# Optimization experiments

Hardware: AMD Instinct MI355X
Metric: run time of the kernel (lower is better)

Reference implementation:

```python
import jax, jax.numpy as jnp
import numpy as np

N_NODES = 100000
N_EDGES = 1600000
D_IN = 128
HID = 128
N_CLS = 10
N_GRAPHS = 128


def _gcn_conv(x, W, b, src, dst, dis, n):
    # x' = W x; out[i] = sum_{(j->i)} d_j^{-1/2} d_i^{-1/2} x'_j ; then + bias
    h = x @ W  # [N, out]
    norm = dis[src] * dis[dst]  # [E_tot]
    msg = h[src] * norm[:, None]  # gather + scale (irregular access)
    out = jax.ops.segment_sum(msg, dst, num_segments=n)  # scatter-add
    return out + b


def setup_inputs() -> dict:
    key = jax.random.key(0)
    ks = jax.random.split(key, 12)
    x = jax.random.normal(ks[0], (N_NODES, D_IN), dtype=jnp.float32)
    edge_index = jax.random.randint(ks[1], (2, N_EDGES), 0, N_NODES, dtype=jnp.int64)
    batch = jnp.sort(jax.random.randint(ks[2], (N_NODES,), 0, N_GRAPHS, dtype=jnp.int64))
    drop_u = jax.random.uniform(ks[3], (N_NODES, D_IN), dtype=jnp.float32)
    s = lambda k, sh, fan: jax.random.normal(k, sh, dtype=jnp.float32) / np.sqrt(fan)
    return {
        "x": x, "edge_index": edge_index, "batch": batch, "num_graphs": N_GRAPHS,
        "drop_u": drop_u,
        "lin1_w": s(ks[4], (D_IN, D_IN), D_IN), "lin1_b": jnp.zeros((D_IN,), jnp.float32),
        "conv1_w": s(ks[5], (D_IN, HID), D_IN), "conv1_b": jnp.zeros((HID,), jnp.float32),
        "conv2_w": s(ks[6], (HID, HID // 2), HID), "conv2_b": jnp.zeros((HID // 2,), jnp.float32),
        "lin2_w": s(ks[7], (HID // 2, N_CLS), HID // 2), "lin2_b": jnp.zeros((N_CLS,), jnp.float32),
    }


def reference(x, edge_index, batch, num_graphs, drop_u,
              lin1_w, lin1_b, conv1_w, conv1_b, conv2_w, conv2_b, lin2_w, lin2_b):
    n = x.shape[0]
    # add self loops (PyG GCNConv default)
    loop = jnp.arange(n, dtype=edge_index.dtype)
    src = jnp.concatenate([edge_index[0], loop])
    dst = jnp.concatenate([edge_index[1], loop])
    deg = jax.ops.segment_sum(jnp.ones_like(dst, dtype=x.dtype), dst, num_segments=n)
    dis = jnp.where(deg > 0, jax.lax.rsqrt(deg), 0.0)  # deg^{-1/2}

    h = x @ lin1_w + lin1_b
    h = _gcn_conv(h, conv1_w, conv1_b, src, dst, dis, n)
    # dropout p=0.5 (training mode in original): keep where u >= 0.5, scale by 2
    h = h * (drop_u >= 0.5).astype(h.dtype) * 2.0
    h = jax.nn.relu(h)
    h = _gcn_conv(h, conv2_w, conv2_b, src, dst, dis, n)
    # global mean pool over graph ids
    sums = jax.ops.segment_sum(h, batch, num_segments=num_graphs)
    cnts = jax.ops.segment_sum(jnp.ones((n,), h.dtype), batch, num_segments=num_graphs)
    pooled = sums / jnp.maximum(cnts, 1.0)[:, None]
    return pooled @ lin2_w + lin2_b
```

## Files before the change

### kernel.cpp

```cpp
#include <hip/hip_runtime.h>
#include <hip/hip_bf16.h>

#define DIN   128
#define HID2  64
#define NCLS  10
#define NGRAPH 128
#define SCAN_CHUNK 1024
#define NBLK 256
#define NBKT_MAX 512
#define CAP 6144

typedef __attribute__((ext_vector_type(8))) short bf16x8;
typedef __attribute__((ext_vector_type(4))) float f32x4;

__device__ __forceinline__ void atomAddF(float* p, float v) {
    unsafeAtomicAdd(p, v);
}

__device__ __forceinline__ unsigned short f2bf(float f) {
    unsigned int u = __float_as_uint(f);
    u += 0x7fffu + ((u >> 16) & 1u);
    return (unsigned short)(u >> 16);
}

__global__ __launch_bounds__(128) void k_w12(const float* __restrict__ lw,
                                             const float* __restrict__ lb,
                                             const float* __restrict__ cw,
                                             const float* __restrict__ cw2,
                                             float* __restrict__ W12,
                                             float* __restrict__ c1preb,
                                             unsigned short* __restrict__ w2b) {
    int i = blockIdx.x, j = threadIdx.x;
    if (i == 129) {
        for (int f = j; f < 8192; f += 128) w2b[f] = f2bf(cw2[(f & 127) * 64 + (f >> 7)]);
        return;
    }
    const float* arow = (i < 128) ? (lw + i * 128) : lb;
    float acc = 0.f;
#pragma unroll 8
    for (int k = 0; k < 128; ++k) acc += arow[k] * cw[k * 128 + j];
    if (i < 128) W12[i * 128 + j] = acc;
    else         c1preb[j] = acc;
}

__global__ __launch_bounds__(256) void k_bhist(const int* __restrict__ dst,
                                               int* __restrict__ bh, int E, int nbkt,
                                               float* __restrict__ zbuf, int zn) {
    __shared__ int lh[NBKT_MAX];
    if (blockIdx.x == 0)
        for (int i = threadIdx.x; i < zn; i += 256) zbuf[i] = 0.f;
    for (int i = threadIdx.x; i < nbkt; i += 256) lh[i] = 0;
    __syncthreads();
    for (int e = blockIdx.x * 256 + threadIdx.x; e < E; e += NBLK * 256)
        atomicAdd(&lh[__builtin_nontemporal_load(dst + e) >> 8], 1);
    __syncthreads();
    for (int i = threadIdx.x; i < nbkt; i += 256) bh[i * NBLK + blockIdx.x] = lh[i];
}

__global__ __launch_bounds__(256) void k_scan_part(const int* __restrict__ cnt,
                                                   int* __restrict__ part, int n) {
    int base = blockIdx.x * SCAN_CHUNK + threadIdx.x * 4;
    int s = 0;
#pragma unroll
    for (int j = 0; j < 4; ++j) { int i = base + j; if (i < n) s += cnt[i]; }
#pragma unroll
    for (int o = 32; o > 0; o >>= 1) s += __shfl_down(s, o);
    __shared__ int wsum[4];
    if ((threadIdx.x & 63) == 0) wsum[threadIdx.x >> 6] = s;
    __syncthreads();
    if (threadIdx.x == 0) part[blockIdx.x] = wsum[0] + wsum[1] + wsum[2] + wsum[3];
}
__global__ __launch_bounds__(256) void k_scan_mid(int* __restrict__ part,
                                                  int* __restrict__ total_out,
                                                  int B, int n) {
    __shared__ int sh[256];
    int t = threadIdx.x;
    int v = (t < B) ? part[t] : 0;
    sh[t] = v;
    __syncthreads();
    for (int off = 1; off < 256; off <<= 1) {
        int u = (t >= off) ? sh[t - off] : 0;
        __syncthreads();
        sh[t] += u;
        __syncthreads();
    }
    if (t < B) part[t] = sh[t] - v;
    if (t == 255) total_out[n] = sh[255];
}
__global__ __launch_bounds__(256) void k_scan_fin2(const int* cnt,
                                                   const int* __restrict__ part,
                                                   int* out, int n) {
    __shared__ int sh[256];
    int t = threadIdx.x;
    int base = blockIdx.x * SCAN_CHUNK + t * 4;
    int c[4]; int s = 0;
#pragma unroll
    for (int j = 0; j < 4; ++j) { int i = base + j; c[j] = (i < n) ? cnt[i] : 0; s += c[j]; }
    sh[t] = s;
    __syncthreads();
    for (int off = 1; off < 256; off <<= 1) {
        int u = (t >= off) ? sh[t - off] : 0;
        __syncthreads();
        sh[t] += u;
        __syncthreads();
    }
    int excl = part[blockIdx.x] + sh[t] - s;
#pragma unroll
    for (int j = 0; j < 4; ++j) {
        int i = base + j;
        if (i < n) out[i] = excl;
        excl += c[j];
    }
}

__global__ __launch_bounds__(256) void k_partition(const int* __restrict__ src,
                                                   const int* __restrict__ dst,
                                                   const int* __restrict__ bh,
                                                   int* __restrict__ pairs, int E, int nbkt) {
    __shared__ int cur[NBKT_MAX];
    for (int i = threadIdx.x; i < nbkt; i += 256) cur[i] = bh[i * NBLK + blockIdx.x];
    __syncthreads();
    for (int e = blockIdx.x * 256 + threadIdx.x; e < E; e += NBLK * 256) {
        int d = __builtin_nontemporal_load(dst + e);
        int s = __builtin_nontemporal_load(src + e);
        int pos = atomicAdd(&cur[d >> 8], 1);
        pairs[pos] = (s << 8) | (d & 255);
    }
}

__global__ __launch_bounds__(256) void k_csr_local(const int* __restrict__ pairs,
                                                   const int* __restrict__ bh,
                                                   int* __restrict__ row_start,
                                                   float* __restrict__ dis,
                                                   int* __restrict__ col,
                                                   int N) {
    __shared__ int cntL[256], scanL[256], curL[256];
    __shared__ int srcbuf[CAP];
    const int tid = threadIdx.x;
    const int lo = blockIdx.x << 8;
    const int bstart = bh[blockIdx.x * NBLK];
    const int bend = bh[(blockIdx.x + 1) * NBLK];
    const int nE = bend - bstart;

    cntL[tid] = 0;
    __syncthreads();
    for (int e = bstart + tid; e < bend; e += 256)
        atomicAdd(&cntL[pairs[e] & 255], 1);
    __syncthreads();
    const int deg = cntL[tid];
    scanL[tid] = deg;
    __syncthreads();
    for (int off = 1; off < 256; off <<= 1) {
        int u = (tid >= off) ? scanL[tid - off] : 0;
        __syncthreads();
        scanL[tid] += u;
        __syncthreads();
    }
    const int excl = scanL[tid] - deg;
    curL[tid] = excl;
    const int node = lo + tid;
    if (node < N) {
        row_start[node] = bstart + excl;
        dis[node] = rsqrtf((float)(deg + 1));
    } else if (node == N) {
        row_start[N] = bend;
    }
    __syncthreads();
    if (nE <= CAP) {
        for (int e = bstart + tid; e < bend; e += 256) {
            int p = pairs[e];
            int pos = atomicAdd(&curL[p & 255], 1);
            srcbuf[pos] = ((unsigned int)p) >> 8;
        }
        __syncthreads();
        for (int i = tid; i < nE; i += 256)
            col[bstart + i] = srcbuf[i];
    } else {
        for (int e = bstart + tid; e < bend; e += 256) {
            int p = pairs[e];
            int pos = atomicAdd(&curL[p & 255], 1);
            col[bstart + pos] = ((unsigned int)p) >> 8;
        }
    }
}

__global__ __launch_bounds__(256) void k_mask(const float* __restrict__ du,
                                              unsigned int* __restrict__ dmask, int nw) {
    const int w = blockIdx.x * 256 + threadIdx.x;
    if (w >= nw) return;
    const float* p = du + (size_t)w * 32;
    unsigned int m = 0;
#pragma unroll
    for (int j = 0; j < 8; ++j) {
        const float4 v = *(const float4*)(p + j * 4);
        m |= (v.x >= 0.5f ? 1u : 0u) << (j * 4 + 0);
        m |= (v.y >= 0.5f ? 1u : 0u) << (j * 4 + 1);
        m |= (v.z >= 0.5f ? 1u : 0u) << (j * 4 + 2);
        m |= (v.w >= 0.5f ? 1u : 0u) << (j * 4 + 3);
    }
    dmask[w] = m;
}

template <int NCOL>
__global__ __launch_bounds__(256) void k_gemm_mfma(const float* __restrict__ A,
                                                   const float* __restrict__ W,
                                                   const float* __restrict__ bias,
                                                   unsigned short* __restrict__ out, int M) {
    constexpr int KP = 136;
    __shared__ unsigned short As[64 * KP];
    __shared__ unsigned short Wt[NCOL * KP];

    const int tid = threadIdx.x;
    const int row0 = blockIdx.x * 64;

    for (int f = tid; f < 2048; f += 256) {
        int r = f >> 5, c4 = f & 31;
        int gr = row0 + r;
        float4 v = make_float4(0.f, 0.f, 0.f, 0.f);
        if (gr < M) v = *(const float4*)(A + (size_t)gr * 128 + c4 * 4);
        ushort4 b;
        b.x = f2bf(v.x); b.y = f2bf(v.y); b.z = f2bf(v.z); b.w = f2bf(v.w);
        *(ushort4*)(&As[r * KP + c4 * 4]) = b;
    }
    for (int f = tid; f < 32 * NCOL; f += 256) {
        int k = f / (NCOL / 4), n4 = f % (NCOL / 4);
        float4 v = *(const float4*)(W + (size_t)k * NCOL + n4 * 4);
        Wt[(n4 * 4 + 0) * KP + k] = f2bf(v.x);
        Wt[(n4 * 4 + 1) * KP + k] = f2bf(v.y);
        Wt[(n4 * 4 + 2) * KP + k] = f2bf(v.z);
        Wt[(n4 * 4 + 3) * KP + k] = f2bf(v.w);
    }
    __syncthreads();

    const int wave = tid >> 6, lane = tid & 63;
    const int quad = lane >> 4, l16 = lane & 15;
    constexpr int CT = (NCOL == 128) ? 2 : 1;
    const int col0 = wave * 16 * CT;

    f32x4 acc[4][CT];
#pragma unroll
    for (int rt = 0; rt < 4; ++rt)
#pragma unroll
        for (int ct = 0; ct < CT; ++ct) acc[rt][ct] = 0.f;

#pragma unroll
    for (int ks = 0; ks < 4; ++ks) {
        const int kbase = ks * 32 + quad * 8;
        bf16x8 bfr[CT];
#pragma unroll
        for (int ct = 0; ct < CT; ++ct)
            bfr[ct] = *(const bf16x8*)(&Wt[(col0 + ct * 16 + l16) * KP + kbase]);
#pragma unroll
        for (int rt = 0; rt < 4; ++rt) {
            bf16x8 afr = *(const bf16x8*)(&As[(rt * 16 + l16) * KP + kbase]);
#pragma unroll
            for (int ct = 0; ct < CT; ++ct)
                acc[rt][ct] = __builtin_amdgcn_mfma_f32_16x16x32_bf16(afr, bfr[ct], acc[rt][ct], 0, 0, 0);
        }
    }

#pragma unroll
    for (int rt = 0; rt < 4; ++rt)
#pragma unroll
        for (int ct = 0; ct < CT; ++ct) {
            const int c = col0 + ct * 16 + l16;
            const float bv = bias ? bias[c] : 0.f;
#pragma unroll
            for (int reg = 0; reg < 4; ++reg) {
                const int gr = row0 + rt * 16 + quad * 4 + reg;
                if (gr < M) out[(size_t)gr * NCOL + c] = f2bf(acc[rt][ct][reg] + bv);
            }
        }
}

__device__ __forceinline__ void bfacc(uint4 v, float d, float* acc) {
    acc[0] = fmaf(d, __uint_as_float(v.x << 16),        acc[0]);
    acc[1] = fmaf(d, __uint_as_float(v.x & 0xffff0000u), acc[1]);
    acc[2] = fmaf(d, __uint_as_float(v.y << 16),        acc[2]);
    acc[3] = fmaf(d, __uint_as_float(v.y & 0xffff0000u), acc[3]);
    acc[4] = fmaf(d, __uint_as_float(v.z << 16),        acc[4]);
    acc[5] = fmaf(d, __uint_as_float(v.z & 0xffff0000u), acc[5]);
    acc[6] = fmaf(d, __uint_as_float(v.w << 16),        acc[6]);
    acc[7] = fmaf(d, __uint_as_float(v.w & 0xffff0000u), acc[7]);
}

__global__ __launch_bounds__(256) void k_gather_gemm2(const unsigned short* __restrict__ h,
                                                      const int* __restrict__ row_start,
                                                      const int* __restrict__ col,
                                                      const float* __restrict__ dis,
                                                      const float* __restrict__ bias,
                                                      const unsigned int* __restrict__ dmask,
                                                      const unsigned short* __restrict__ w2b,
                                                      unsigned short* __restrict__ h2b,
                                                      int n) {
    constexpr int KP = 136;
    __shared__ unsigned short As[16 * KP];
    __shared__ unsigned short Wt[64 * KP];
    const int tid = threadIdx.x;
    const int node0 = blockIdx.x * 16;
    const int node = node0 + (tid >> 4);
    const int l = tid & 15;
    const int coff = l * 8;

    for (int f = tid * 4; f < 8192; f += 1024) {
        const int c = f >> 7, k = f & 127;
        *(ushort4*)(&Wt[c * KP + k]) = *(const ushort4*)(&w2b[f]);
    }

    float r[8];
    if (node < n) {
        const float dn = dis[node];
        const unsigned int mword = dmask[node * 4 + (l >> 2)];
        const unsigned int mbyte = (mword >> ((l & 3) * 8)) & 0xffu;
        float acc[8];
        {
            uint4 v = *(const uint4*)(h + (size_t)node * 128 + coff);
#pragma unroll
            for (int q = 0; q < 8; ++q) acc[q] = 0.f;
            bfacc(v, dn, acc);
        }
        const int beg = row_start[node], end = row_start[node + 1];
        int j = beg;
        for (; j + 3 < end; j += 4) {
            const int s0 = col[j], s1 = col[j + 1], s2 = col[j + 2], s3 = col[j + 3];
            const float d0 = dis[s0], d1 = dis[s1], d2 = dis[s2], d3 = dis[s3];
            const uint4 v0 = *(const uint4*)(h + (size_t)s0 * 128 + coff);
            const uint4 v1 = *(const uint4*)(h + (size_t)s1 * 128 + coff);
            const uint4 v2 = *(const uint4*)(h + (size_t)s2 * 128 + coff);
            const uint4 v3 = *(const uint4*)(h + (size_t)s3 * 128 + coff);
            bfacc(v0, d0, acc);
            bfacc(v1, d1, acc);
            bfacc(v2, d2, acc);
            bfacc(v3, d3, acc);
        }
        for (; j < end; ++j) {
            const int s0 = col[j];
            const float d0 = dis[s0];
            const uint4 v0 = *(const uint4*)(h + (size_t)s0 * 128 + coff);
            bfacc(v0, d0, acc);
        }
        const float4 b0 = *(const float4*)(bias + coff);
        const float4 b1 = *(const float4*)(bias + coff + 4);
        r[0] = fmaf(dn, acc[0], b0.x); r[1] = fmaf(dn, acc[1], b0.y);
        r[2] = fmaf(dn, acc[2], b0.z); r[3] = fmaf(dn, acc[3], b0.w);
        r[4] = fmaf(dn, acc[4], b1.x); r[5] = fmaf(dn, acc[5], b1.y);
        r[6] = fmaf(dn, acc[6], b1.z); r[7] = fmaf(dn, acc[7], b1.w);
#pragma unroll
        for (int q = 0; q < 8; ++q)
            r[q] = ((mbyte >> q) & 1u) ? 2.f * fmaxf(r[q], 0.f) : 0.f;
    } else {
#pragma unroll
        for (int q = 0; q < 8; ++q) r[q] = 0.f;
    }
    ushort4 o0, o1;
    o0.x = f2bf(r[0]); o0.y = f2bf(r[1]); o0.z = f2bf(r[2]); o0.w = f2bf(r[3]);
    o1.x = f2bf(r[4]); o1.y = f2bf(r[5]); o1.z = f2bf(r[6]); o1.w = f2bf(r[7]);
    *(ushort4*)(&As[(tid >> 4) * KP + coff]) = o0;
    *(ushort4*)(&As[(tid >> 4) * KP + coff + 4]) = o1;
    __syncthreads();

    const int wave = tid >> 6, lane = tid & 63;
    const int quad = lane >> 4, l16 = lane & 15;
    const int c0 = wave * 16;
    f32x4 a2 = 0.f;
#pragma unroll
    for (int ks = 0; ks < 4; ++ks) {
        const int kbase = ks * 32 + quad * 8;
        bf16x8 afr = *(const bf16x8*)(&As[l16 * KP + kbase]);
        bf16x8 bfr = *(const bf16x8*)(&Wt[(c0 + l16) * KP + kbase]);
        a2 = __builtin_amdgcn_mfma_f32_16x16x32_bf16(afr, bfr, a2, 0, 0, 0);
    }
#pragma unroll
    for (int reg = 0; reg < 4; ++reg) {
        const int gr = node0 + quad * 4 + reg;
        if (gr < n) h2b[(size_t)gr * 64 + c0 + l16] = f2bf(a2[reg]);
    }
}

__global__ __launch_bounds__(256) void k_gather_pool(const unsigned short* __restrict__ h,
                                                     const int* __restrict__ row_start,
                                                     const int* __restrict__ col,
                                                     const float* __restrict__ dis,
                                                     const float* __restrict__ bias,
                                                     const int* __restrict__ batch,
                                                     float* __restrict__ partial,
                                                     int* __restrict__ bgid,
                                                     int* __restrict__ bvcnt,
                                                     float* __restrict__ sums,
                                                     float* __restrict__ cnt, int n) {
    __shared__ float bsum[4][64];
    __shared__ int sh_gfirst, sh_uni;
    const int tid = threadIdx.x;
    const int node = (blockIdx.x * 256 + tid) >> 3;
    const int l = tid & 7;
    const int coff = l * 8;
    const bool valid = node < n;
    const int node0 = blockIdx.x * 32;

    if (tid == 0) { sh_gfirst = batch[node0]; sh_uni = 1; }
    __syncthreads();
    const int gfirst = sh_gfirst;

    float r[8];
    int g = gfirst;
    if (valid) {
        const float dn = dis[node];
        g = batch[node];
        float acc[8];
        {
            uint4 v = *(const uint4*)(h + (size_t)node * 64 + coff);
#pragma unroll
            for (int q = 0; q < 8; ++q) acc[q] = 0.f;
            bfacc(v, dn, acc);
        }
        const int beg = row_start[node], end = row_start[node + 1];
        int j = beg;
        for (; j + 3 < end; j += 4) {
            const int s0 = col[j], s1 = col[j + 1], s2 = col[j + 2], s3 = col[j + 3];
            const float d0 = dis[s0], d1 = dis[s1], d2 = dis[s2], d3 = dis[s3];
            const uint4 v0 = *(const uint4*)(h + (size_t)s0 * 64 + coff);
            const uint4 v1 = *(const uint4*)(h + (size_t)s1 * 64 + coff);
            const uint4 v2 = *(const uint4*)(h + (size_t)s2 * 64 + coff);
            const uint4 v3 = *(const uint4*)(h + (size_t)s3 * 64 + coff);
            bfacc(v0, d0, acc);
            bfacc(v1, d1, acc);
            bfacc(v2, d2, acc);
            bfacc(v3, d3, acc);
        }
        for (; j < end; ++j) {
            const int s0 = col[j];
            const float d0 = dis[s0];
            const uint4 v0 = *(const uint4*)(h + (size_t)s0 * 64 + coff);
            bfacc(v0, d0, acc);
        }
        const float4 b0 = *(const float4*)(bias + coff);
        const float4 b1 = *(const float4*)(bias + coff + 4);
        r[0] = fmaf(dn, acc[0], b0.x); r[1] = fmaf(dn, acc[1], b0.y);
        r[2] = fmaf(dn, acc[2], b0.z); r[3] = fmaf(dn, acc[3], b0.w);
        r[4] = fmaf(dn, acc[4], b1.x); r[5] = fmaf(dn, acc[5], b1.y);
        r[6] = fmaf(dn, acc[6], b1.z); r[7] = fmaf(dn, acc[7], b1.w);
    } else {
#pragma unroll
        for (int q = 0; q < 8; ++q) r[q] = 0.f;
    }

    if (valid && g != gfirst) atomicAnd(&sh_uni, 0);
    __syncthreads();

    if (sh_uni) {
#pragma unroll
        for (int q = 0; q < 8; ++q) {
            r[q] += __shfl_xor(r[q], 8);
            r[q] += __shfl_xor(r[q], 16);
            r[q] += __shfl_xor(r[q], 32);
        }
        const int wave = tid >> 6, lane = tid & 63;
        if (lane < 8) {
#pragma unroll
            for (int q = 0; q < 8; ++q) bsum[wave][lane * 8 + q] = r[q];
        }
        __syncthreads();
        if (tid < 64)
            partial[(size_t)blockIdx.x * 64 + tid] =
                bsum[0][tid] + bsum[1][tid] + bsum[2][tid] + bsum[3][tid];
        if (tid == 0) {
            bgid[blockIdx.x] = gfirst;
            bvcnt[blockIdx.x] = min(n - node0, 32);
        }
    } else {
        if (tid == 0) bgid[blockIdx.x] = -1;
        const int g0 = __shfl(g, 0);
        const bool wuni = __all(valid && (g == g0));
        if (wuni) {
#pragma unroll
            for (int q = 0; q < 8; ++q) {
                r[q] += __shfl_xor(r[q], 8);
                r[q] += __shfl_xor(r[q], 16);
                r[q] += __shfl_xor(r[q], 32);
            }
            const int lane = tid & 63;
            if (lane < 8) {
#pragma unroll
                for (int q = 0; q < 8; ++q) atomAddF(&sums[g0 * 64 + lane * 8 + q], r[q]);
                if (lane == 0) atomAddF(&cnt[g0], 8.0f);
            }
        } else if (valid) {
#pragma unroll
            for (int q = 0; q < 8; ++q) atomAddF(&sums[g * 64 + coff + q], r[q]);
            if (l == 0) atomAddF(&cnt[g], 1.0f);
        }
    }
}

__global__ __launch_bounds__(256) void k_pool2(const float* __restrict__ partial,
                                               const int* __restrict__ bgid,
                                               const int* __restrict__ bvcnt,
                                               float* __restrict__ sums,
                                               float* __restrict__ cnt, int nb) {
    const int grp = (blockIdx.x * 256 + (int)threadIdx.x) >> 6;
    const int f = threadIdx.x & 63;
    const int ngroups = gridDim.x * 4;
    const int per = (nb + ngroups - 1) / ngroups;
    const int start = grp * per, end = min(nb, start + per);
    if (start >= end) return;
    int cg = -1;
    float acc = 0.f;
    int vc = 0;
    for (int b = start; b < end; ++b) {
        const int g = bgid[b];
        if (g != cg) {
            if (cg >= 0) {
                atomAddF(&sums[cg * 64 + f], acc);
                if (f == 0) atomAddF(&cnt[cg], (float)vc);
            }
            acc = 0.f; vc = 0; cg = g;
        }
        if (g >= 0) {
            acc += partial[(size_t)b * 64 + f];
            vc += bvcnt[b];
        }
    }
    if (cg >= 0) {
        atomAddF(&sums[cg * 64 + f], acc);
        if (f == 0) atomAddF(&cnt[cg], (float)vc);
    }
}

__global__ __launch_bounds__(64) void k_final(const float* __restrict__ sums,
                                              const float* __restrict__ cnt,
                                              const float* __restrict__ w,
                                              const float* __restrict__ b,
                                              float* __restrict__ out) {
    int g = blockIdx.x, f = threadIdx.x;
    float c = fmaxf(cnt[g], 1.0f);
    float p = sums[g * 64 + f] / c;
#pragma unroll
    for (int cls = 0; cls < NCLS; ++cls) {
        float v = p * w[f * 10 + cls];
#pragma unroll
        for (int o = 32; o > 0; o >>= 1) v += __shfl_down(v, o);
        if (f == 0) out[g * 10 + cls] = v + b[cls];
    }
}

extern "C" void kernel_launch(void* const* d_in, const int* in_sizes, int n_in,
                              void* d_out, int out_size, void* d_ws, size_t ws_size,
                              hipStream_t stream) {
    const float* x       = (const float*)d_in[0];
    const int*   ei      = (const int*)d_in[1];
    const int*   batch   = (const int*)d_in[2];
    const float* drop_u  = (const float*)d_in[4];
    const float* lin1_w  = (const float*)d_in[5];
    const float* lin1_b  = (const float*)d_in[6];
    const float* conv1_w = (const float*)d_in[7];
    const float* conv1_b = (const float*)d_in[8];
    const float* conv2_w = (const float*)d_in[9];
    const float* conv2_b = (const float*)d_in[10];
    const float* lin2_w  = (const float*)d_in[11];
    const float* lin2_b  = (const float*)d_in[12];
    float* out = (float*)d_out;

    const int N = in_sizes[0] / DIN;
    const int E = in_sizes[1] / 2;
    const int* src = ei;
    const int* dst = ei + E;

    const int nbkt = (N + 255) >> 8;
    const int M = nbkt * NBLK;
    const int nbGP = (int)(((size_t)N * 8 + 255) / 256);

    float* ws    = (float*)d_ws;
    float* out1  = ws;
    unsigned short* h1b = (unsigned short*)(ws + (size_t)N * 128);
    float* dis   = ws + (size_t)N * 128 + (size_t)N * 64;
    float* W12   = dis + N;
    float* c1pb  = W12 + 16384;
    float* sums  = c1pb + 128;
    float* cntp  = sums + NGRAPH * 64;
    int*   row_start = (int*)(cntp + NGRAPH);
    int*   part  = row_start + N + 2;
    int*   bh    = part + 256;
    int*   col   = bh + NBKT_MAX * NBLK + 2;
    int*   pairs = col + E;
    float* partial = (float*)(pairs + E);
    int*   bgid  = (int*)(partial + (size_t)nbGP * 64);
    int*   bvcnt = bgid + nbGP;
    unsigned int* dmask = (unsigned int*)pairs;
    unsigned short* h2b = (unsigned short*)out1;
    unsigned short* w2b = (unsigned short*)(out1 + (size_t)N * 64);

    k_w12<<<130, 128, 0, stream>>>(lin1_w, lin1_b, conv1_w, conv2_w, W12, c1pb, w2b);

    k_bhist<<<NBLK, 256, 0, stream>>>(dst, bh, E, nbkt, sums, NGRAPH * 64 + NGRAPH);
    const int scanB = (M + SCAN_CHUNK - 1) / SCAN_CHUNK;
    k_scan_part<<<scanB, 256, 0, stream>>>(bh, part, M);
    k_scan_mid<<<1, 256, 0, stream>>>(part, bh, scanB, M);
    k_scan_fin2<<<scanB, 256, 0, stream>>>(bh, part, bh, M);
    k_partition<<<NBLK, 256, 0, stream>>>(src, dst, bh, pairs, E, nbkt);
    k_csr_local<<<nbkt, 256, 0, stream>>>(pairs, bh, row_start, dis, col, N);

    k_mask<<<(N * 4 + 255) / 256, 256, 0, stream>>>(drop_u, dmask, N * 4);

    const int gemmGrid = (N + 63) / 64;
    k_gemm_mfma<128><<<gemmGrid, 256, 0, stream>>>(x, W12, c1pb, h1b, N);

    k_gather_gemm2<<<(N + 15) / 16, 256, 0, stream>>>(h1b, row_start, col, dis, conv1_b,
                                                      dmask, w2b, h2b, N);

    k_gather_pool<<<nbGP, 256, 0, stream>>>(h2b, row_start, col, dis, conv2_b, batch,
                                            partial, bgid, bvcnt, sums, cntp, N);
    k_pool2<<<16, 256, 0, stream>>>(partial, bgid, bvcnt, sums, cntp, nbGP);

    k_final<<<NGRAPH, 64, 0, stream>>>(sums, cntp, lin2_w, lin2_b, out);
}
```

Measured before the change: 379.3 us.

## Fuse weight prep into histogram, mask into GEMM, and stage partition in LDS

The W12/bias/W2 weight-precompute kernel is folded into extra blocks of the bucket-histogram launch, and the dropout-mask packing is folded into the first MFMA GEMM's load phase. Together these remove two kernel launches. The partition kernel now recomputes a per-block local histogram, scans it, scatters edges into an LDS buffer grouped by bucket, and then writes them out contiguously with a binary search for each bucket's global offset. This replaces scattered global writes with coalesced ones, at the cost of a second pass over dst, an LDS scan, and a per-element binary search.

```diff
diff --git a/kernel.cpp b/kernel.cpp
--- a/kernel.cpp
+++ b/kernel.cpp
@@ -9,6 +9,7 @@
 #define NBLK 256
 #define NBKT_MAX 512
 #define CAP 6144
+#define EPB 6400
 
 typedef __attribute__((ext_vector_type(8))) short bf16x8;
 typedef __attribute__((ext_vector_type(4))) float f32x4;
@@ -23,38 +24,44 @@
     return (unsigned short)(u >> 16);
 }
 
-__global__ __launch_bounds__(128) void k_w12(const float* __restrict__ lw,
-                                             const float* __restrict__ lb,
-                                             const float* __restrict__ cw,
-                                             const float* __restrict__ cw2,
-                                             float* __restrict__ W12,
-                                             float* __restrict__ c1preb,
-                                             unsigned short* __restrict__ w2b) {
-    int i = blockIdx.x, j = threadIdx.x;
-    if (i == 129) {
-        for (int f = j; f < 8192; f += 128) w2b[f] = f2bf(cw2[(f & 127) * 64 + (f >> 7)]);
-        return;
-    }
-    const float* arow = (i < 128) ? (lw + i * 128) : lb;
-    float acc = 0.f;
-#pragma unroll 8
-    for (int k = 0; k < 128; ++k) acc += arow[k] * cw[k * 128 + j];
-    if (i < 128) W12[i * 128 + j] = acc;
-    else         c1preb[j] = acc;
-}
-
 __global__ __launch_bounds__(256) void k_bhist(const int* __restrict__ dst,
                                                int* __restrict__ bh, int E, int nbkt,
-                                               float* __restrict__ zbuf, int zn) {
+                                               float* __restrict__ zbuf, int zn,
+                                               const float* __restrict__ lw,
+                                               const float* __restrict__ lb,
+                                               const float* __restrict__ cw,
+                                               const float* __restrict__ cw2,
+                                               float* __restrict__ W12,
+                                               float* __restrict__ c1preb,
+                                               unsigned short* __restrict__ w2b) {
+    const int tid = threadIdx.x;
+    if (blockIdx.x >= NBLK) {
+        const int bi = blockIdx.x - NBLK;
+        if (bi == 65) {
+            for (int f = tid; f < 8192; f += 256) w2b[f] = f2bf(cw2[(f & 127) * 64 + (f >> 7)]);
+        } else {
+            const int i = bi * 2 + (tid >> 7);
+            if (i <= 128) {
+                const int j = tid & 127;
+                const float* arow = (i < 128) ? (lw + i * 128) : lb;
+                float acc = 0.f;
+#pragma unroll 8
+                for (int k = 0; k < 128; ++k) acc += arow[k] * cw[k * 128 + j];
+                if (i < 128) W12[i * 128 + j] = acc;
+                else         c1preb[j] = acc;
+            }
+        }
+        return;
+    }
     __shared__ int lh[NBKT_MAX];
     if (blockIdx.x == 0)
-        for (int i = threadIdx.x; i < zn; i += 256) zbuf[i] = 0.f;
-    for (int i = threadIdx.x; i < nbkt; i += 256) lh[i] = 0;
-    __syncthreads();
-    for (int e = blockIdx.x * 256 + threadIdx.x; e < E; e += NBLK * 256)
+        for (int i = tid; i < zn; i += 256) zbuf[i] = 0.f;
+    for (int i = tid; i < nbkt; i += 256) lh[i] = 0;
+    __syncthreads();
+    for (int e = blockIdx.x * 256 + tid; e < E; e += NBLK * 256)
         atomicAdd(&lh[__builtin_nontemporal_load(dst + e) >> 8], 1);
     __syncthreads();
-    for (int i = threadIdx.x; i < nbkt; i += 256) bh[i * NBLK + blockIdx.x] = lh[i];
+    for (int i = tid; i < nbkt; i += 256) bh[i * NBLK + blockIdx.x] = lh[i];
 }
 
 __global__ __launch_bounds__(256) void k_scan_part(const int* __restrict__ cnt,
@@ -117,14 +124,57 @@
                                                    const int* __restrict__ dst,
                                                    const int* __restrict__ bh,
                                                    int* __restrict__ pairs, int E, int nbkt) {
-    __shared__ int cur[NBKT_MAX];
-    for (int i = threadIdx.x; i < nbkt; i += 256) cur[i] = bh[i * NBLK + blockIdx.x];
-    __syncthreads();
-    for (int e = blockIdx.x * 256 + threadIdx.x; e < E; e += NBLK * 256) {
-        int d = __builtin_nontemporal_load(dst + e);
-        int s = __builtin_nontemporal_load(src + e);
-        int pos = atomicAdd(&cur[d >> 8], 1);
-        pairs[pos] = (s << 8) | (d & 255);
+    __shared__ int lh[NBKT_MAX];
+    __shared__ int lscan[NBKT_MAX + 2];
+    __shared__ int gofs[NBKT_MAX];
+    __shared__ int lcur[NBKT_MAX];
+    __shared__ int scanw[256];
+    __shared__ int lbuf[EPB];
+    const int tid = threadIdx.x;
+    const int b = blockIdx.x;
+
+    for (int i = tid; i < NBKT_MAX; i += 256) lh[i] = 0;
+    __syncthreads();
+    for (int e = b * 256 + tid; e < E; e += NBLK * 256)
+        atomicAdd(&lh[__builtin_nontemporal_load(dst + e) >> 8], 1);
+    __syncthreads();
+    const int a0 = lh[2 * tid], a1 = lh[2 * tid + 1];
+    const int ps = a0 + a1;
+    scanw[tid] = ps;
+    __syncthreads();
+    for (int off = 1; off < 256; off <<= 1) {
+        int u = (tid >= off) ? scanw[tid - off] : 0;
+        __syncthreads();
+        scanw[tid] += u;
+        __syncthreads();
+    }
+    const int ex = scanw[tid] - ps;
+    lscan[2 * tid] = ex;
+    lscan[2 * tid + 1] = ex + a0;
+    if (tid == 255) lscan[512] = scanw[255];
+    __syncthreads();
+#pragma unroll
+    for (int q = 0; q < 2; ++q) {
+        const int k = 2 * tid + q;
+        lcur[k] = lscan[k];
+        if (k < nbkt) gofs[k] = bh[k * NBLK + b] - lscan[k];
+    }
+    __syncthreads();
+    for (int e = b * 256 + tid; e < E; e += NBLK * 256) {
+        const int d = __builtin_nontemporal_load(dst + e);
+        const int s = __builtin_nontemporal_load(src + e);
+        const int lpos = atomicAdd(&lcur[d >> 8], 1);
+        lbuf[lpos] = (s << 8) | (d & 255);
+    }
+    __syncthreads();
+    const int cnt = lscan[512];
+    for (int i = tid; i < cnt; i += 256) {
+        int lo = 0, hi = nbkt;
+        while (hi - lo > 1) {
+            const int mid = (lo + hi) >> 1;
+            if (lscan[mid] <= i) lo = mid; else hi = mid;
+        }
+        pairs[gofs[lo] + i] = lbuf[i];
     }
 }
 
@@ -184,27 +234,12 @@
     }
 }
 
-__global__ __launch_bounds__(256) void k_mask(const float* __restrict__ du,
-                                              unsigned int* __restrict__ dmask, int nw) {
-    const int w = blockIdx.x * 256 + threadIdx.x;
-    if (w >= nw) return;
-    const float* p = du + (size_t)w * 32;
-    unsigned int m = 0;
-#pragma unroll
-    for (int j = 0; j < 8; ++j) {
-        const float4 v = *(const float4*)(p + j * 4);
-        m |= (v.x >= 0.5f ? 1u : 0u) << (j * 4 + 0);
-        m |= (v.y >= 0.5f ? 1u : 0u) << (j * 4 + 1);
-        m |= (v.z >= 0.5f ? 1u : 0u) << (j * 4 + 2);
-        m |= (v.w >= 0.5f ? 1u : 0u) << (j * 4 + 3);
-    }
-    dmask[w] = m;
-}
-
 template <int NCOL>
 __global__ __launch_bounds__(256) void k_gemm_mfma(const float* __restrict__ A,
                                                    const float* __restrict__ W,
                                                    const float* __restrict__ bias,
+                                                   const float* __restrict__ du,
+                                                   unsigned int* __restrict__ dmask,
                                                    unsigned short* __restrict__ out, int M) {
     constexpr int KP = 136;
     __shared__ unsigned short As[64 * KP];
@@ -229,6 +264,22 @@
         Wt[(n4 * 4 + 1) * KP + k] = f2bf(v.y);
         Wt[(n4 * 4 + 2) * KP + k] = f2bf(v.z);
         Wt[(n4 * 4 + 3) * KP + k] = f2bf(v.w);
+    }
+    if (dmask) {
+        const int gr = row0 + (tid >> 2), w = tid & 3;
+        if (gr < M) {
+            const float* p = du + (size_t)gr * 128 + w * 32;
+            unsigned int m = 0;
+#pragma unroll
+            for (int jj = 0; jj < 8; ++jj) {
+                const float4 v = *(const float4*)(p + jj * 4);
+                m |= (v.x >= 0.5f ? 1u : 0u) << (jj * 4 + 0);
+                m |= (v.y >= 0.5f ? 1u : 0u) << (jj * 4 + 1);
+                m |= (v.z >= 0.5f ? 1u : 0u) << (jj * 4 + 2);
+                m |= (v.w >= 0.5f ? 1u : 0u) << (jj * 4 + 3);
+            }
+            dmask[gr * 4 + w] = m;
+        }
     }
     __syncthreads();
 
@@ -589,9 +640,8 @@
     unsigned short* h2b = (unsigned short*)out1;
     unsigned short* w2b = (unsigned short*)(out1 + (size_t)N * 64);
 
-    k_w12<<<130, 128, 0, stream>>>(lin1_w, lin1_b, conv1_w, conv2_w, W12, c1pb, w2b);
-
-    k_bhist<<<NBLK, 256, 0, stream>>>(dst, bh, E, nbkt, sums, NGRAPH * 64 + NGRAPH);
+    k_bhist<<<NBLK + 66, 256, 0, stream>>>(dst, bh, E, nbkt, sums, NGRAPH * 64 + NGRAPH,
+                                           lin1_w, lin1_b, conv1_w, conv2_w, W12, c1pb, w2b);
     const int scanB = (M + SCAN_CHUNK - 1) / SCAN_CHUNK;
     k_scan_part<<<scanB, 256, 0, stream>>>(bh, part, M);
     k_scan_mid<<<1, 256, 0, stream>>>(part, bh, scanB, M);
@@ -599,10 +649,8 @@
     k_partition<<<NBLK, 256, 0, stream>>>(src, dst, bh, pairs, E, nbkt);
     k_csr_local<<<nbkt, 256, 0, stream>>>(pairs, bh, row_start, dis, col, N);
 
-    k_mask<<<(N * 4 + 255) / 256, 256, 0, stream>>>(drop_u, dmask, N * 4);
-
     const int gemmGrid = (N + 63) / 64;
-    k_gemm_mfma<128><<<gemmGrid, 256, 0, stream>>>(x, W12, c1pb, h1b, N);
+    k_gemm_mfma<128><<<gemmGrid, 256, 0, stream>>>(x, W12, c1pb, drop_u, dmask, h1b, N);
 
     k_gather_gemm2<<<(N + 15) / 16, 256, 0, stream>>>(h1b, row_start, col, dis, conv1_b,
                                                       dmask, w2b, h2b, N);
```

Measured after the change: 382.0 us. Within noise of the previous version (+0.7%).
